# Performance work log

Hardware: AMD Instinct MI355X
Metric: run time of the kernel (lower is better)

Reference implementation:

```python
import jax, jax.numpy as jnp
import numpy as np

MIN_DISTANCE = 31  # glimpse size (h, w)


def setup_inputs() -> dict:
    key = jax.random.key(0)
    k1, k2, k3 = jax.random.split(key, 3)
    B, N, C, H, W = 8, 600, 32, 256, 256
    images = jax.random.normal(k1, (B, C, H, W), dtype=jnp.float32)
    # anchor boxes (xmin, ymin, xmax, ymax) in pixel coords, kept in-bounds
    xy1 = jax.random.uniform(k2, (B, N, 2), dtype=jnp.float32) * (H - 64) + 16.0
    wh = jax.random.uniform(k3, (B, N, 2), dtype=jnp.float32) * 32.0 + 8.0
    anc_bases = jnp.concatenate([xy1, xy1 + wh], axis=-1)  # [B, N, 4]
    return {"images": images, "anc_bases": anc_bases}


def _grid_sample_bilinear_zeros(images, grid):
    """torch.nn.functional.grid_sample(mode='bilinear', padding_mode='zeros',
    align_corners=False), vectorized over an arbitrary flat sample dim.
    images: [B, C, H, W]; grid: [B, P, 2] normalized coords (x, y) in [-1, 1].
    Returns [B, C, P].
    """
    B, C, H, W = images.shape
    # unnormalize (align_corners=False)
    px = (grid[..., 0] + 1.0) * (W * 0.5) - 0.5  # [B, P]
    py = (grid[..., 1] + 1.0) * (H * 0.5) - 0.5
    x0 = jnp.floor(px)
    y0 = jnp.floor(py)
    fx = px - x0
    fy = py - y0
    x0i = x0.astype(jnp.int32)
    y0i = y0.astype(jnp.int32)
    x1i = x0i + 1
    y1i = y0i + 1

    imgf = images.reshape(B, C, H * W)

    def corner(yi, xi, wgt):
        valid = (yi >= 0) & (yi < H) & (xi >= 0) & (xi < W)
        yc = jnp.clip(yi, 0, H - 1)
        xc = jnp.clip(xi, 0, W - 1)
        idx = (yc * W + xc)[:, None, :]  # [B, 1, P]
        vals = jnp.take_along_axis(imgf, idx, axis=2)  # [B, C, P]
        w_eff = jnp.where(valid, wgt, 0.0)[:, None, :]
        return vals * w_eff

    out = (
        corner(y0i, x0i, (1.0 - fx) * (1.0 - fy))
        + corner(y0i, x1i, fx * (1.0 - fy))
        + corner(y1i, x0i, (1.0 - fx) * fy)
        + corner(y1i, x1i, fx * fy)
    )
    return out  # [B, C, P]


def _extract_glimpses(images, anc_centers, size):
    B, C, H, W = images.shape
    N = anc_centers.shape[1]
    h, w = size
    xs = jnp.arange(w, dtype=images.dtype) - (w - 1) / 2.0
    ys = jnp.arange(h, dtype=images.dtype) - (h - 1) / 2.0
    vy, vx = jnp.meshgrid(ys, xs, indexing="ij")  # [h, w]
    grid = jnp.stack([vx, vy], axis=-1)  # [h, w, 2] (x, y)
    # offsets_grid: [B, N, h, w, 2]
    og = anc_centers[:, :, None, None, :] + grid[None, None, ...]
    norm = jnp.asarray([W / 2.0, H / 2.0], dtype=images.dtype)
    g = (og - norm) / norm  # normalized for grid_sample
    g_flat = g.reshape(B, N * h * w, 2)
    out = _grid_sample_bilinear_zeros(images, g_flat)  # [B, C, N*h*w]
    rois = out.reshape(B, C, N, h, w).transpose(0, 2, 1, 3, 4)  # [B, N, C, h, w]
    return rois


def reference(images, anc_bases):
    # eval path of CornerProposal.forward (targets=None)
    # note original: (a[..., :2] + a[..., :2]) // 2 == floor(a[..., :2])
    anc_centers = (anc_bases[:, :, :2] + anc_bases[:, :, :2]) // 2.0
    rois = _extract_glimpses(
        images, anc_centers, size=(MIN_DISTANCE, MIN_DISTANCE)
    )
    return rois, anc_bases[:, :, :2]
```

## Files before the change

kernel.cpp:

```cpp
#include <hip/hip_runtime.h>

#define BB 8
#define NN 600
#define CC 32
#define HH 256
#define WW 256
#define GG 31
#define PP 32
#define PATCH (PP * PP)

__global__ __launch_bounds__(256) void rois_kernel(const float* __restrict__ images,
                                                   const float* __restrict__ anc,
                                                   float* __restrict__ out,
                                                   float* __restrict__ out_anc) {
    __shared__ float lds[4][2][PATCH];
    const int bn   = blockIdx.x;
    const int b    = bn / NN;
    const int t    = threadIdx.x;
    const int wave = t >> 6;
    const int lane = t & 63;

    const float ax = anc[bn * 4 + 0];
    const float ay = anc[bn * 4 + 1];
    const int x0 = (int)floorf(ax) - 16;
    const int y0 = (int)floorf(ay) - 16;

    if (t == 0) {
        out_anc[bn * 2 + 0] = ax;
        out_anc[bn * 2 + 1] = ay;
    }

    const int lrow = lane >> 5;
    const int lcol = lane & 31;
    const size_t plane = (size_t)HH * WW;
    const float* imgbase = images + (size_t)(b * CC) * plane
                         + (size_t)(y0 + lrow) * WW + (x0 + lcol);
    float* outbase = out + (size_t)bn * CC * (GG * GG);

    float pre[16];

    {
        const float* ip = imgbase + (size_t)wave * plane;
        #pragma unroll
        for (int k = 0; k < 16; ++k)
            pre[k] = ip[(size_t)(2 * k) * WW];
        float* sb = lds[wave][0];
        #pragma unroll
        for (int k = 0; k < 16; ++k)
            sb[lane + 64 * k] = pre[k];
    }

    #pragma unroll 1
    for (int it = 0; it < 8; ++it) {
        const int c = wave + 4 * it;

        if (it + 1 < 8) {
            const float* ip = imgbase + (size_t)(c + 4) * plane;
            #pragma unroll
            for (int k = 0; k < 16; ++k)
                pre[k] = ip[(size_t)(2 * k) * WW];
        }

        const float* sb = lds[wave][it & 1];
        float* o = outbase + (size_t)c * (GG * GG);
        if (lcol < GG) {
            #pragma unroll
            for (int k = 0; k < 16; ++k) {
                const int row = 2 * k + lrow;
                if (row < GG) {
                    const float* sp = sb + row * PP + lcol;
                    o[row * GG + lcol] =
                        0.25f * (sp[0] + sp[1] + sp[PP] + sp[PP + 1]);
                }
            }
        }

        if (it + 1 < 8) {
            float* sb2 = lds[wave][(it + 1) & 1];
            #pragma unroll
            for (int k = 0; k < 16; ++k)
                sb2[lane + 64 * k] = pre[k];
        }
    }
}

extern "C" void kernel_launch(void* const* d_in, const int* in_sizes, int n_in,
                              void* d_out, int out_size, void* d_ws, size_t ws_size,
                              hipStream_t stream) {
    const float* images = (const float*)d_in[0];
    const float* anc    = (const float*)d_in[1];
    float* out = (float*)d_out;
    float* out_anchors = out + (size_t)BB * NN * CC * GG * GG;

    rois_kernel<<<BB * NN, 256, 0, stream>>>(images, anc, out, out_anchors);
}
```

Measured before the change: 709.7 us.

## Stage glimpse patches with direct global-to-LDS loads, cooperating per channel

Replaces the per-wave register prefetch and LDS store with __builtin_amdgcn_global_load_lds, so global data goes straight into a double-buffered shared patch. All four waves now work together on one channel at a time, with a block barrier after each channel. The block index is remapped to interleave anchors across groups, outputs use nontemporal stores, and launch bounds ask for 8 blocks per CU. The goal is to cut VGPR pressure and LDS write instructions and to raise occupancy. The cost is 32 block-wide barriers per block.

Result: faster. 691.2 us (-2.6%).

```diff
diff --git a/kernel.cpp b/kernel.cpp
--- a/kernel.cpp
+++ b/kernel.cpp
@@ -9,16 +9,24 @@
 #define PP 32
 #define PATCH (PP * PP)
 
-__global__ __launch_bounds__(256) void rois_kernel(const float* __restrict__ images,
-                                                   const float* __restrict__ anc,
-                                                   float* __restrict__ out,
-                                                   float* __restrict__ out_anc) {
-    __shared__ float lds[4][2][PATCH];
-    const int bn   = blockIdx.x;
-    const int b    = bn / NN;
+
+typedef __attribute__((address_space(3))) void lds_void_t;
+typedef const __attribute__((address_space(1))) void gmem_void_t;
+
+__global__ __launch_bounds__(256, 8) void rois_kernel(const float* __restrict__ images,
+                                                      const float* __restrict__ anc,
+                                                      float* __restrict__ out,
+                                                      float* __restrict__ out_anc) {
+    __shared__ float patch[2][PATCH];
+
+    const int bid = blockIdx.x;
+    const int bn  = (bid & 7) * ((BB * NN) / 8) + (bid >> 3);
+    const int b   = bn / NN;
+
     const int t    = threadIdx.x;
     const int wave = t >> 6;
-    const int lane = t & 63;
+    const int tr   = t >> 5;
+    const int lcol = t & 31;
 
     const float ax = anc[bn * 4 + 0];
     const float ay = anc[bn * 4 + 1];
@@ -30,57 +38,48 @@
         out_anc[bn * 2 + 1] = ay;
     }
 
-    const int lrow = lane >> 5;
-    const int lcol = lane & 31;
     const size_t plane = (size_t)HH * WW;
-    const float* imgbase = images + (size_t)(b * CC) * plane
-                         + (size_t)(y0 + lrow) * WW + (x0 + lcol);
+    const float* gbase = images + (size_t)(b * CC) * plane
+                       + (size_t)(y0 + tr) * WW + (x0 + lcol);
     float* outbase = out + (size_t)bn * CC * (GG * GG);
 
-    float pre[16];
-
     {
-        const float* ip = imgbase + (size_t)wave * plane;
+        float* sb = &patch[0][64 * wave];
         #pragma unroll
-        for (int k = 0; k < 16; ++k)
-            pre[k] = ip[(size_t)(2 * k) * WW];
-        float* sb = lds[wave][0];
-        #pragma unroll
-        for (int k = 0; k < 16; ++k)
-            sb[lane + 64 * k] = pre[k];
+        for (int k = 0; k < 4; ++k)
+            __builtin_amdgcn_global_load_lds((gmem_void_t*)(gbase + (size_t)(8 * k) * WW),
+                                             (lds_void_t*)(sb + 256 * k),
+                                             4, 0, 0);
     }
+    __syncthreads();
 
     #pragma unroll 1
-    for (int it = 0; it < 8; ++it) {
-        const int c = wave + 4 * it;
-
-        if (it + 1 < 8) {
-            const float* ip = imgbase + (size_t)(c + 4) * plane;
+    for (int c = 0; c < CC; ++c) {
+        if (c + 1 < CC) {
+            const float* gp = gbase + (size_t)(c + 1) * plane;
+            float* sb2 = &patch[(c + 1) & 1][64 * wave];
             #pragma unroll
-            for (int k = 0; k < 16; ++k)
-                pre[k] = ip[(size_t)(2 * k) * WW];
+            for (int k = 0; k < 4; ++k)
+                __builtin_amdgcn_global_load_lds((gmem_void_t*)(gp + (size_t)(8 * k) * WW),
+                                                 (lds_void_t*)(sb2 + 256 * k),
+                                                 4, 0, 0);
         }
 
-        const float* sb = lds[wave][it & 1];
+        const float* sb = patch[c & 1];
         float* o = outbase + (size_t)c * (GG * GG);
         if (lcol < GG) {
             #pragma unroll
-            for (int k = 0; k < 16; ++k) {
-                const int row = 2 * k + lrow;
-                if (row < GG) {
-                    const float* sp = sb + row * PP + lcol;
-                    o[row * GG + lcol] =
-                        0.25f * (sp[0] + sp[1] + sp[PP] + sp[PP + 1]);
+            for (int k = 0; k < 4; ++k) {
+                const int r = 8 * k + tr;
+                if (r < GG) {
+                    const float* sp = sb + r * PP + lcol;
+                    const float v = 0.25f * (sp[0] + sp[1] + sp[PP] + sp[PP + 1]);
+                    __builtin_nontemporal_store(v, &o[r * GG + lcol]);
                 }
             }
         }
 
-        if (it + 1 < 8) {
-            float* sb2 = lds[wave][(it + 1) & 1];
-            #pragma unroll
-            for (int k = 0; k < 16; ++k)
-                sb2[lane + 64 * k] = pre[k];
-        }
+        __syncthreads();
     }
 }
 
```
